# Kernel tuning notes

Hardware: AMD Instinct MI355X
Metric: run time of the kernel (lower is better)

The kernel has to match this reference:

```python
import jax, jax.numpy as jnp
import numpy as np

K = 8
TEMP = 0.05
EPS = 1e-8


def setup_inputs() -> dict:
    key = jax.random.key(0)
    k1, k2, k3, k4, k5, k6 = jax.random.split(key, 6)
    N, D, H = 8192, 1024, 64
    h0 = jax.random.normal(k1, (N, D), dtype=jnp.float32)
    coords = jax.random.uniform(k2, (N, 2), dtype=jnp.float32)
    # tiny MLP params: Linear(2,H) -> ReLU -> Linear(H,1) -> Sigmoid
    W1 = jax.random.normal(k3, (2, H), dtype=jnp.float32) * (1.0 / np.sqrt(2))
    b1 = jnp.zeros((H,), dtype=jnp.float32)
    W2 = jax.random.normal(k4, (H, 1), dtype=jnp.float32) * (1.0 / np.sqrt(H))
    b2 = jnp.zeros((1,), dtype=jnp.float32)
    return {"h0": h0, "coords": coords, "W1": W1, "b1": b1, "W2": W2, "b2": b2}


def reference(h0, coords, W1, b1, W2, b2):
    # pairwise euclidean distances [N, N]
    sq = jnp.sum(coords * coords, axis=-1)                      # [N]
    d2 = sq[:, None] + sq[None, :] - 2.0 * (coords @ coords.T)  # [N, N]
    dist = jnp.sqrt(jnp.maximum(d2, 0.0))

    # k+1 nearest (smallest dist), drop self (index 0)
    _, idx = jax.lax.top_k(-dist, K + 1)                        # [N, K+1]
    knn_idx = idx[:, 1:]                                        # [N, K]

    # gather neighbor features [N, K, D]
    neighbor_feats = h0[knn_idx]

    # cosine similarity between h_i and each neighbor (torch eps semantics)
    num = jnp.einsum('nd,nkd->nk', h0, neighbor_feats)          # [N, K]
    ni = jnp.maximum(jnp.linalg.norm(h0, axis=-1), EPS)         # [N]
    nj = jnp.maximum(jnp.linalg.norm(neighbor_feats, axis=-1), EPS)  # [N, K]
    sim = num / (ni[:, None] * nj)

    # spatial weights from gathered distances
    d_knn = jnp.take_along_axis(dist, knn_idx, axis=1)          # [N, K]
    spatial_w = jnp.exp(-d_knn / TEMP)

    density_input = jnp.stack(
        [sim.mean(axis=1), spatial_w.mean(axis=1)], axis=1)     # [N, 2]

    hmid = jax.nn.relu(density_input @ W1 + b1)
    density = jax.nn.sigmoid(hmid @ W2 + b2)                    # [N, 1]
    return density
```

## Files before the change

kernel.cpp:

```cpp
#include <hip/hip_runtime.h>
#include <math.h>

#define NROWS 8192
#define DIM   1024
#define GRID  64
#define CELLW 0.015625f
#define LPR   16

__device__ __forceinline__ int cell_of(float v) {
    int c = (int)(v * 64.0f);
    return c < 0 ? 0 : (c > 63 ? 63 : c);
}

__device__ __forceinline__ float np_d2(float xi, float yi, float sqi,
                                       float xj, float yj) {
    float sqj = __fadd_rn(__fmul_rn(xj, xj), __fmul_rn(yj, yj));
    float G   = fmaf(yi, yj, __fmul_rn(xi, xj));
    return __fsub_rn(__fadd_rn(sqi, sqj), __fmul_rn(2.0f, G));
}

__global__ __launch_bounds__(1024) void build_grid_kernel(
    const float* __restrict__ coords,
    int* __restrict__ cellStart,
    float4* __restrict__ sxyz) {

    __shared__ int lcnt[4096];
    __shared__ int wsum[16];
    const int t = threadIdx.x;

    for (int i = t; i < 4096; i += 1024) lcnt[i] = 0;
    __syncthreads();

    float2 pc[8]; int pcell[8];
#pragma unroll
    for (int k = 0; k < 8; ++k) {
        int i = t + 1024 * k;
        float2 c = ((const float2*)coords)[i];
        pc[k] = c;
        pcell[k] = cell_of(c.y) * GRID + cell_of(c.x);
        atomicAdd(&lcnt[pcell[k]], 1);
    }
    __syncthreads();

    int c0 = lcnt[t*4+0], c1 = lcnt[t*4+1], c2 = lcnt[t*4+2], c3 = lcnt[t*4+3];
    int s1 = c0, s2 = c0 + c1, s3 = s2 + c2, s4 = s3 + c3;
    int lane = t & 63, wid = t >> 6;
    int inc = s4;
#pragma unroll
    for (int off = 1; off < 64; off <<= 1) {
        int o = __shfl_up(inc, off, 64);
        if (lane >= off) inc += o;
    }
    if (lane == 63) wsum[wid] = inc;
    __syncthreads();
    int wbase = 0;
    for (int w = 0; w < wid; ++w) wbase += wsum[w];
    int excl = wbase + inc - s4;

    cellStart[t*4+0] = excl;
    cellStart[t*4+1] = excl + s1;
    cellStart[t*4+2] = excl + s2;
    cellStart[t*4+3] = excl + s3;
    if (t == 1023) cellStart[4096] = excl + s4;
    lcnt[t*4+0] = excl;
    lcnt[t*4+1] = excl + s1;
    lcnt[t*4+2] = excl + s2;
    lcnt[t*4+3] = excl + s3;
    __syncthreads();

#pragma unroll
    for (int k = 0; k < 8; ++k) {
        int pos = atomicAdd(&lcnt[pcell[k]], 1);
        float x = pc[k].x, y = pc[k].y;
        float sq = __fadd_rn(__fmul_rn(x, x), __fmul_rn(y, y));
        sxyz[pos] = make_float4(x, y, sq, __int_as_float(t + 1024 * k));
    }
}

__global__ __launch_bounds__(256) void knn_kernel(
    const int* __restrict__ cellStart,
    const float4* __restrict__ sxyz,
    unsigned long long* __restrict__ chosen_ws) {

    const int sub = threadIdx.x & (LPR - 1);
    const int g   = (blockIdx.x * 256 + threadIdx.x) / LPR;

    const float4 me = sxyz[g];
    const float xi = me.x, yi = me.y, sqi = me.z;
    const int row = __float_as_int(me.w);
    const int cx = cell_of(xi), cy = cell_of(yi);

    unsigned long long best[10], merged[10];
    int C = 2;
    while (true) {
#pragma unroll
        for (int s = 0; s < 10; ++s) best[s] = ~0ULL;
        int x0 = max(0, cx - C), x1 = min(GRID - 1, cx + C);
        int y0 = max(0, cy - C), y1 = min(GRID - 1, cy + C);
        for (int yy = y0; yy <= y1; ++yy) {
            int s = cellStart[yy * GRID + x0];
            int e = cellStart[yy * GRID + x1 + 1];
            for (int t = s + sub; t < e; t += LPR) {
                float4 c = sxyz[t];
                float d2  = __fsub_rn(__fadd_rn(sqi, c.z),
                                      __fmul_rn(2.0f, fmaf(yi, c.y, __fmul_rn(xi, c.x))));
                float dst = __fsqrt_rn(fmaxf(d2, 0.0f));
                unsigned long long key =
                    ((unsigned long long)__float_as_uint(dst) << 32)
                    | (unsigned int)__float_as_int(c.w);
                if (key < best[9]) {
                    best[9] = key;
#pragma unroll
                    for (int ss = 9; ss >= 1; --ss) {
                        unsigned long long a = best[ss - 1], b = best[ss];
                        unsigned long long lo = a < b ? a : b;
                        unsigned long long hi = a < b ? b : a;
                        best[ss - 1] = lo;
                        best[ss]     = hi;
                    }
                }
            }
        }
#pragma unroll
        for (int r = 0; r < 10; ++r) {
            unsigned long long mn = best[0];
#pragma unroll
            for (int off = 1; off < LPR; off <<= 1) {
                unsigned long long o = __shfl_xor(mn, off, 64);
                mn = (o < mn) ? o : mn;
            }
            if (best[0] == mn) {
#pragma unroll
                for (int ss = 0; ss < 9; ++ss) best[ss] = best[ss + 1];
                best[9] = ~0ULL;
            }
            merged[r] = mn;
        }
        bool done = false;
        if (merged[9] != ~0ULL) {
            float d9 = __uint_as_float((unsigned int)(merged[9] >> 32));
            if (d9 + 1.0e-3f <= (float)C * CELLW) done = true;
        }
        if (done || C >= GRID) break;
        C <<= 1; if (C > GRID) C = GRID;
    }

    if (sub == 0) {
        unsigned long long* o = chosen_ws + (size_t)row * 10;
#pragma unroll
        for (int r = 0; r < 10; ++r) o[r] = merged[r];
    }
}

__global__ __launch_bounds__(256) void gather_kernel(
    const float* __restrict__ h0,
    const unsigned long long* __restrict__ chosen_ws,
    const float4* __restrict__ sxyz,
    float* __restrict__ pdot,
    float* __restrict__ norms) {

    const int wid  = threadIdx.x >> 6;
    const int lane = threadIdx.x & 63;
    const int bid  = blockIdx.x;
    const int grp  = (bid & 7) * (NROWS / 8) + (bid >> 3);
    const int row  = __float_as_int(sxyz[grp].w);

    const unsigned long long* ch = chosen_ws + (size_t)row * 10;
    const float4* hi = (const float4*)(h0 + (size_t)row * DIM);

    const int s0 = wid, s1 = wid + 4, s2 = wid + 8;
    const bool nbr2  = (wid <= 1);
    const bool self2 = (wid == 2);

    const int j0 = (int)(ch[s0] & 0xFFFFFFFFu);
    const int j1 = (int)(ch[s1] & 0xFFFFFFFFu);
    const int j2 = nbr2 ? (int)(ch[s2] & 0xFFFFFFFFu) : 0;

    const float4* b0p = (const float4*)(h0 + (size_t)j0 * DIM);
    const float4* b1p = (const float4*)(h0 + (size_t)j1 * DIM);
    const float4* b2p = (const float4*)(h0 + (size_t)j2 * DIM);

    float4 av[4], bv0[4], bv1[4], bv2[4];
#pragma unroll
    for (int t = 0; t < 4; ++t) {
        av[t]  = hi [lane + 64 * t];
        bv0[t] = b0p[lane + 64 * t];
        bv1[t] = b1p[lane + 64 * t];
    }
    if (nbr2) {
#pragma unroll
        for (int t = 0; t < 4; ++t) bv2[t] = b2p[lane + 64 * t];
    }

    float p0 = 0.f, p1 = 0.f, p2 = 0.f;
#pragma unroll
    for (int t = 0; t < 4; ++t) {
        p0 += av[t].x * bv0[t].x + av[t].y * bv0[t].y + av[t].z * bv0[t].z + av[t].w * bv0[t].w;
        p1 += av[t].x * bv1[t].x + av[t].y * bv1[t].y + av[t].z * bv1[t].z + av[t].w * bv1[t].w;
    }
    if (nbr2) {
#pragma unroll
        for (int t = 0; t < 4; ++t)
            p2 += av[t].x * bv2[t].x + av[t].y * bv2[t].y + av[t].z * bv2[t].z + av[t].w * bv2[t].w;
    } else if (self2) {
#pragma unroll
        for (int t = 0; t < 4; ++t)
            p2 += av[t].x * av[t].x + av[t].y * av[t].y + av[t].z * av[t].z + av[t].w * av[t].w;
    }

#pragma unroll
    for (int off = 1; off < 64; off <<= 1) {
        p0 += __shfl_xor(p0, off, 64);
        p1 += __shfl_xor(p1, off, 64);
        p2 += __shfl_xor(p2, off, 64);
    }

    if (lane == 0) {
        float* pr = pdot + (size_t)row * 10;
        pr[s0] = p0;
        pr[s1] = p1;
        if (nbr2)  pr[s2] = p2;
        if (self2) norms[row] = sqrtf(p2);
    }
}

__global__ __launch_bounds__(256) void final_kernel(
    const float* __restrict__ coords,
    const unsigned long long* __restrict__ chosen_ws,
    const float* __restrict__ pdot,
    const float* __restrict__ norms,
    const float* __restrict__ W1, const float* __restrict__ b1,
    const float* __restrict__ W2, const float* __restrict__ b2,
    float* __restrict__ out) {

    const int widx = threadIdx.x >> 6;
    const int lane = threadIdx.x & 63;
    const int row  = blockIdx.x * 4 + widx;

    const float2 ci = ((const float2*)coords)[row];
    const float xi = ci.x, yi = ci.y;
    const float sqi = __fadd_rn(__fmul_rn(xi, xi), __fmul_rn(yi, yi));

    unsigned long long chosen[10];
    const unsigned long long* ch = chosen_ws + (size_t)row * 10;
#pragma unroll
    for (int r = 0; r < 10; ++r) chosen[r] = ch[r];

    auto clamped_d2 = [&](unsigned long long key) -> float {
        int j = (int)(key & 0xFFFFFFFFu);
        float2 cj = ((const float2*)coords)[j];
        return fmaxf(np_d2(xi, yi, sqi, cj.x, cj.y), 0.0f);
    };
    const float m0 = clamped_d2(chosen[0]);
    const float m1 = clamped_d2(chosen[1]);
    const float m2 = clamped_d2(chosen[2]);
    const float m8 = clamped_d2(chosen[8]);
    const float m9 = clamped_d2(chosen[9]);

    const float WIN = 2.0e-6f;
    const bool fpair = (m1 - m0) <= WIN;
    const bool ftri  = fpair && ((m2 - m0) <= WIN);
    const bool f89   = (m9 - m8) <= WIN;

    float wd[3];
    wd[0] = ftri ? (1.f / 3.f) : (fpair ? 0.5f : 1.0f);
    wd[1] = ftri ? (1.f / 3.f) : (fpair ? 0.5f : 0.0f);
    wd[2] = ftri ? (1.f / 3.f) : 0.0f;
    const float wc0 = f89 ? 0.5f : 1.0f;
    const float wc1 = f89 ? 0.5f : 0.0f;

    const float ni = fmaxf(norms[row], 1e-8f);

    float sim[10], sw[10];
#pragma unroll
    for (int r = 0; r < 10; ++r) {
        int   j   = (int)(chosen[r] & 0xFFFFFFFFu);
        float dst = __uint_as_float((unsigned int)(chosen[r] >> 32));
        float nj  = fmaxf(norms[j], 1e-8f);
        sim[r] = pdot[(size_t)row * 10 + r] / (ni * nj);
        sw[r]  = expf(__fdiv_rn(-dst, 0.05f));
    }

    float Ssim = 0.f, Ssw = 0.f;
#pragma unroll
    for (int r = 0; r < 9; ++r) { Ssim += sim[r]; Ssw += sw[r]; }

    const float w1a = W1[lane], w1b = W1[64 + lane];
    const float b1l = b1[lane], w2l = W2[lane], b2s = b2[0];

    float outacc = 0.f;
#pragma unroll
    for (int d = 0; d < 3; ++d) {
#pragma unroll
        for (int c = 0; c < 2; ++c) {
            float wgt = wd[d] * (c ? wc1 : wc0);
            float simsum = Ssim - sim[d] + (c ? (sim[9] - sim[8]) : 0.f);
            float swsum  = Ssw  - sw[d]  + (c ? (sw[9]  - sw[8])  : 0.f);
            float di0 = simsum * 0.125f;
            float di1 = swsum  * 0.125f;
            float hm = fmaxf(di0 * w1a + di1 * w1b + b1l, 0.f);
            float v  = hm * w2l;
#pragma unroll
            for (int off = 1; off < 64; off <<= 1) v += __shfl_xor(v, off, 64);
            float z = v + b2s;
            outacc += wgt * (1.f / (1.f + expf(-z)));
        }
    }

    if (lane == 0) out[row] = outacc;
}

extern "C" void kernel_launch(void* const* d_in, const int* in_sizes, int n_in,
                              void* d_out, int out_size, void* d_ws, size_t ws_size,
                              hipStream_t stream) {
    const float* h0     = (const float*)d_in[0];
    const float* coords = (const float*)d_in[1];
    const float* W1     = (const float*)d_in[2];
    const float* b1     = (const float*)d_in[3];
    const float* W2     = (const float*)d_in[4];
    const float* b2     = (const float*)d_in[5];
    float* out = (float*)d_out;

    char* ws = (char*)d_ws;
    unsigned long long* chosen_ws = (unsigned long long*)(ws);
    float*  pdot      = (float*)(ws + 655360);
    float*  norms     = (float*)(ws + 983040);
    float4* sxyz      = (float4*)(ws + 1015808);
    int*    cellStart = (int*)(ws + 1146880);

    build_grid_kernel<<<1, 1024, 0, stream>>>(coords, cellStart, sxyz);
    knn_kernel       <<<NROWS * LPR / 256, 256, 0, stream>>>(cellStart, sxyz, chosen_ws);
    gather_kernel    <<<NROWS, 256, 0, stream>>>(h0, chosen_ws, sxyz, pdot, norms);
    final_kernel     <<<NROWS / 4, 256, 0, stream>>>(coords, chosen_ws, pdot, norms,
                                                     W1, b1, W2, b2, out);
}
```

Baseline: 60.06 us.

## Split single-block grid build into parallel count, scan and scatter kernels

Replaces the one-block build_grid kernel, which binned all 8192 points on a single CU, with a memset, a multi-block count kernel using global atomics, a single-block scan, and a multi-block scatter kernel. The aim is to spread the binning and scatter across many CUs instead of serialising them on one block. In exchange it adds three extra launches plus a memset, and uses global rather than LDS atomics. Scatter order within a cell becomes nondeterministic, which may change tie-breaking in the neighbour search.

```diff
diff --git a/kernel.cpp b/kernel.cpp
--- a/kernel.cpp
+++ b/kernel.cpp
@@ -19,30 +19,19 @@
     return __fsub_rn(__fadd_rn(sqi, sqj), __fmul_rn(2.0f, G));
 }
 
-__global__ __launch_bounds__(1024) void build_grid_kernel(
-    const float* __restrict__ coords,
-    int* __restrict__ cellStart,
-    float4* __restrict__ sxyz) {
-
-    __shared__ int lcnt[4096];
+__global__ __launch_bounds__(256) void count_kernel(const float* __restrict__ coords,
+                                                    int* __restrict__ cnt) {
+    int i = blockIdx.x * 256 + threadIdx.x;
+    float2 c = ((const float2*)coords)[i];
+    atomicAdd(cnt + cell_of(c.y) * GRID + cell_of(c.x), 1);
+}
+
+__global__ __launch_bounds__(1024) void scan_kernel(const int* __restrict__ cnt,
+                                                    int* __restrict__ start,
+                                                    int* __restrict__ cur) {
     __shared__ int wsum[16];
-    const int t = threadIdx.x;
-
-    for (int i = t; i < 4096; i += 1024) lcnt[i] = 0;
-    __syncthreads();
-
-    float2 pc[8]; int pcell[8];
-#pragma unroll
-    for (int k = 0; k < 8; ++k) {
-        int i = t + 1024 * k;
-        float2 c = ((const float2*)coords)[i];
-        pc[k] = c;
-        pcell[k] = cell_of(c.y) * GRID + cell_of(c.x);
-        atomicAdd(&lcnt[pcell[k]], 1);
-    }
-    __syncthreads();
-
-    int c0 = lcnt[t*4+0], c1 = lcnt[t*4+1], c2 = lcnt[t*4+2], c3 = lcnt[t*4+3];
+    int t = threadIdx.x;
+    int c0 = cnt[t * 4 + 0], c1 = cnt[t * 4 + 1], c2 = cnt[t * 4 + 2], c3 = cnt[t * 4 + 3];
     int s1 = c0, s2 = c0 + c1, s3 = s2 + c2, s4 = s3 + c3;
     int lane = t & 63, wid = t >> 6;
     int inc = s4;
@@ -56,25 +45,22 @@
     int wbase = 0;
     for (int w = 0; w < wid; ++w) wbase += wsum[w];
     int excl = wbase + inc - s4;
-
-    cellStart[t*4+0] = excl;
-    cellStart[t*4+1] = excl + s1;
-    cellStart[t*4+2] = excl + s2;
-    cellStart[t*4+3] = excl + s3;
-    if (t == 1023) cellStart[4096] = excl + s4;
-    lcnt[t*4+0] = excl;
-    lcnt[t*4+1] = excl + s1;
-    lcnt[t*4+2] = excl + s2;
-    lcnt[t*4+3] = excl + s3;
-    __syncthreads();
-
-#pragma unroll
-    for (int k = 0; k < 8; ++k) {
-        int pos = atomicAdd(&lcnt[pcell[k]], 1);
-        float x = pc[k].x, y = pc[k].y;
-        float sq = __fadd_rn(__fmul_rn(x, x), __fmul_rn(y, y));
-        sxyz[pos] = make_float4(x, y, sq, __int_as_float(t + 1024 * k));
-    }
+    start[t * 4 + 0] = excl;        cur[t * 4 + 0] = excl;
+    start[t * 4 + 1] = excl + s1;   cur[t * 4 + 1] = excl + s1;
+    start[t * 4 + 2] = excl + s2;   cur[t * 4 + 2] = excl + s2;
+    start[t * 4 + 3] = excl + s3;   cur[t * 4 + 3] = excl + s3;
+    if (t == 1023) start[4096] = excl + s4;
+}
+
+__global__ __launch_bounds__(256) void scatter_kernel(const float* __restrict__ coords,
+                                                      int* __restrict__ cur,
+                                                      float4* __restrict__ sxyz) {
+    int i = blockIdx.x * 256 + threadIdx.x;
+    float2 c = ((const float2*)coords)[i];
+    int cell = cell_of(c.y) * GRID + cell_of(c.x);
+    int pos = atomicAdd(cur + cell, 1);
+    float sq = __fadd_rn(__fmul_rn(c.x, c.x), __fmul_rn(c.y, c.y));
+    sxyz[pos] = make_float4(c.x, c.y, sq, __int_as_float(i));
 }
 
 __global__ __launch_bounds__(256) void knn_kernel(
@@ -327,10 +313,15 @@
     float*  norms     = (float*)(ws + 983040);
     float4* sxyz      = (float4*)(ws + 1015808);
     int*    cellStart = (int*)(ws + 1146880);
-
-    build_grid_kernel<<<1, 1024, 0, stream>>>(coords, cellStart, sxyz);
-    knn_kernel       <<<NROWS * LPR / 256, 256, 0, stream>>>(cellStart, sxyz, chosen_ws);
-    gather_kernel    <<<NROWS, 256, 0, stream>>>(h0, chosen_ws, sxyz, pdot, norms);
-    final_kernel     <<<NROWS / 4, 256, 0, stream>>>(coords, chosen_ws, pdot, norms,
-                                                     W1, b1, W2, b2, out);
-}
+    int*    cellCnt   = (int*)(ws + 1163268);
+    int*    cellCur   = (int*)(ws + 1179652);
+
+    hipMemsetAsync(cellCnt, 0, 4096 * sizeof(int), stream);
+    count_kernel  <<<NROWS / 256, 256, 0, stream>>>(coords, cellCnt);
+    scan_kernel   <<<1, 1024, 0, stream>>>(cellCnt, cellStart, cellCur);
+    scatter_kernel<<<NROWS / 256, 256, 0, stream>>>(coords, cellCur, sxyz);
+    knn_kernel    <<<NROWS * LPR / 256, 256, 0, stream>>>(cellStart, sxyz, chosen_ws);
+    gather_kernel <<<NROWS, 256, 0, stream>>>(h0, chosen_ws, sxyz, pdot, norms);
+    final_kernel  <<<NROWS / 4, 256, 0, stream>>>(coords, chosen_ws, pdot, norms,
+                                                  W1, b1, W2, b2, out);
+}
```

Result: slower. 67.07 us (+11.7%).
